# Optimization experiments

Measured on AMD Instinct MI355X. Metric: run time of the kernel, lower is better.

The kernel has to match this reference:

```python
import jax, jax.numpy as jnp
import numpy as np

N = 4_000_000

# AxisTypes: ZThenX=0, Bisector=1, ZBisect=2, ThreeFold=3, ZOnly=4, NoAxisType=5

def _normv(v):
    return v / jnp.linalg.norm(v, axis=-1, keepdims=True)


def _rot_matrices(coords, z_atoms, x_atoms, y_atoms, axis_types):
    # z axis: toward z neighbor
    z_vec = _normv(coords[z_atoms] - coords)  # (N,3)

    # x vector: gather-based for most types, synthetic for ZOnly/NoAxisType
    fz_only = (axis_types == 4) | (axis_types == 5)
    x_gather = _normv(coords[x_atoms] - coords)
    z0 = z_vec[:, 0:1]
    x_zonly = jnp.concatenate([1.0 - z0, z0, jnp.zeros_like(z0)], axis=1)
    x_vec = jnp.where(fz_only[:, None], x_zonly, x_gather)

    # Bisector: z <- normalize(z + x)
    fb = (axis_types == 1)[:, None]
    z_vec = jnp.where(fb, _normv(z_vec + x_vec), z_vec)

    # y-neighbor direction, used by ZBisect and ThreeFold
    y_nb = _normv(coords[y_atoms] - coords)

    # ZBisect: x <- normalize(x + y_nb)
    fzb = (axis_types == 2)[:, None]
    x_vec = jnp.where(fzb, _normv(x_vec + y_nb), x_vec)

    # ThreeFold: z <- normalize(z + x + y_nb)
    ftf = (axis_types == 3)[:, None]
    z_vec = jnp.where(ftf, _normv(z_vec + x_vec + y_nb), z_vec)

    # Gram-Schmidt orthogonalize x against z, y = z x x
    x_vec = _normv(x_vec - z_vec * jnp.sum(z_vec * x_vec, axis=1, keepdims=True))
    y_vec = jnp.cross(z_vec, x_vec)

    # NoAxisType: identity frame
    fna = (axis_types == 5)[:, None]
    ex = jnp.array([1.0, 0.0, 0.0], coords.dtype)
    ey = jnp.array([0.0, 1.0, 0.0], coords.dtype)
    ez = jnp.array([0.0, 0.0, 1.0], coords.dtype)
    x_vec = jnp.where(fna, ex, x_vec)
    y_vec = jnp.where(fna, ey, y_vec)
    z_vec = jnp.where(fna, ez, z_vec)

    # rows = local X, Y, Z in global coords -> (N,3,3)
    return jnp.stack([x_vec, y_vec, z_vec], axis=1)


def setup_inputs() -> dict:
    key = jax.random.key(0)
    k1, k2, k3, k4, k5, k6, k7 = jax.random.split(key, 7)
    coords = jax.random.normal(k1, (N, 3), jnp.float32) * 10.0
    idx = jnp.arange(N)
    # avoid self-index (zero vector -> NaN in normVec, same as torch original)
    z_atoms = (idx + jax.random.randint(k2, (N,), 1, N)) % N
    x_atoms = (idx + jax.random.randint(k3, (N,), 1, N)) % N
    y_atoms = (idx + jax.random.randint(k4, (N,), 1, N)) % N
    axis_types = jax.random.randint(k5, (N,), 0, 6)
    dipoles = jax.random.normal(k6, (N, 3), jnp.float32)
    quadrupoles = jax.random.normal(k7, (N, 3, 3), jnp.float32)
    return dict(coords=coords, z_atoms=z_atoms, x_atoms=x_atoms,
                y_atoms=y_atoms, axis_types=axis_types,
                dipoles=dipoles, quadrupoles=quadrupoles)


def reference(coords, z_atoms, x_atoms, y_atoms, axis_types, dipoles, quadrupoles):
    rot = _rot_matrices(coords, z_atoms, x_atoms, y_atoms, axis_types)  # (N,3,3)
    # torch: bmm(d.unsqueeze(1), rot).squeeze(1) -> d @ rot
    d = jnp.einsum('nk,nkj->nj', dipoles, rot)
    # torch: rot^T @ q @ rot
    q = jnp.einsum('nki,nkl,nlj->nij', rot, quadrupoles, rot)
    return (d, q)
```

## Files before the change

### kernel.cpp

```cpp
#include <hip/hip_runtime.h>


__device__ __forceinline__ float3 nrm3(float ax, float ay, float az) {
    float s = ax * ax + ay * ay + az * az;
    float r = 1.0f / sqrtf(s);
    return make_float3(ax * r, ay * r, az * r);
}

__device__ __forceinline__ void rot_matrix(
    int t, float cx, float cy, float cz,
    int zi, int xi, int yi,
    const float* __restrict__ coords,
    float R[9])
{
    if (t == 5) {
        R[0] = 1.0f; R[1] = 0.0f; R[2] = 0.0f;
        R[3] = 0.0f; R[4] = 1.0f; R[5] = 0.0f;
        R[6] = 0.0f; R[7] = 0.0f; R[8] = 1.0f;
        return;
    }

    float3 zv = nrm3(coords[3 * zi + 0] - cx,
                     coords[3 * zi + 1] - cy,
                     coords[3 * zi + 2] - cz);

    float3 xv;
    if (t == 4) {
        xv = make_float3(1.0f - zv.x, zv.x, 0.0f);
    } else {
        xv = nrm3(coords[3 * xi + 0] - cx,
                  coords[3 * xi + 1] - cy,
                  coords[3 * xi + 2] - cz);
    }

    if (t == 1) {
        zv = nrm3(zv.x + xv.x, zv.y + xv.y, zv.z + xv.z);
    }

    if (t == 2 || t == 3) {
        float3 yn = nrm3(coords[3 * yi + 0] - cx,
                         coords[3 * yi + 1] - cy,
                         coords[3 * yi + 2] - cz);
        if (t == 2) {
            xv = nrm3(xv.x + yn.x, xv.y + yn.y, xv.z + yn.z);
        } else {
            zv = nrm3(zv.x + xv.x + yn.x, zv.y + xv.y + yn.y, zv.z + xv.z + yn.z);
        }
    }

    float dzx = zv.x * xv.x + zv.y * xv.y + zv.z * xv.z;
    xv = nrm3(xv.x - zv.x * dzx, xv.y - zv.y * dzx, xv.z - zv.z * dzx);

    float3 yv = make_float3(zv.y * xv.z - zv.z * xv.y,
                            zv.z * xv.x - zv.x * xv.z,
                            zv.x * xv.y - zv.y * xv.x);

    R[0] = xv.x; R[1] = xv.y; R[2] = xv.z;
    R[3] = yv.x; R[4] = yv.y; R[5] = yv.z;
    R[6] = zv.x; R[7] = zv.y; R[8] = zv.z;
}

__device__ __forceinline__ void apply_rot(
    const float R[9], const float dp[3], const float Q[9],
    float od[3], float oq[9])
{
    od[0] = dp[0] * R[0] + dp[1] * R[3] + dp[2] * R[6];
    od[1] = dp[0] * R[1] + dp[1] * R[4] + dp[2] * R[7];
    od[2] = dp[0] * R[2] + dp[1] * R[5] + dp[2] * R[8];

    float M[9];
#pragma unroll
    for (int a = 0; a < 3; ++a) {
#pragma unroll
        for (int l = 0; l < 3; ++l) {
            M[a * 3 + l] = R[0 * 3 + a] * Q[0 * 3 + l]
                         + R[1 * 3 + a] * Q[1 * 3 + l]
                         + R[2 * 3 + a] * Q[2 * 3 + l];
        }
    }
#pragma unroll
    for (int a = 0; a < 3; ++a) {
#pragma unroll
        for (int b = 0; b < 3; ++b) {
            oq[a * 3 + b] = M[a * 3 + 0] * R[0 * 3 + b]
                          + M[a * 3 + 1] * R[1 * 3 + b]
                          + M[a * 3 + 2] * R[2 * 3 + b];
        }
    }
}

__global__ __launch_bounds__(256) void mp_rot4_kernel(
    const float* __restrict__ coords,
    const int* __restrict__ za,
    const int* __restrict__ xa,
    const int* __restrict__ ya,
    const int* __restrict__ at,
    const float* __restrict__ dip,
    const float* __restrict__ quad,
    float* __restrict__ out_d,
    float* __restrict__ out_q,
    int ngroups, int n)
{
    int g = blockIdx.x * blockDim.x + threadIdx.x;
    if (g >= ngroups) return;
    int base = 4 * g;

    if (base + 4 <= n) {
        float4 cA = ((const float4*)coords)[3 * g + 0];
        float4 cB = ((const float4*)coords)[3 * g + 1];
        float4 cC = ((const float4*)coords)[3 * g + 2];
        float c[12] = {cA.x, cA.y, cA.z, cA.w, cB.x, cB.y, cB.z, cB.w,
                       cC.x, cC.y, cC.z, cC.w};

        float4 dA = ((const float4*)dip)[3 * g + 0];
        float4 dB = ((const float4*)dip)[3 * g + 1];
        float4 dC = ((const float4*)dip)[3 * g + 2];
        float dp[12] = {dA.x, dA.y, dA.z, dA.w, dB.x, dB.y, dB.z, dB.w,
                        dC.x, dC.y, dC.z, dC.w};

        float q[36];
#pragma unroll
        for (int k = 0; k < 9; ++k) {
            float4 v = ((const float4*)quad)[9 * g + k];
            q[4 * k + 0] = v.x; q[4 * k + 1] = v.y;
            q[4 * k + 2] = v.z; q[4 * k + 3] = v.w;
        }

        int4 z4 = ((const int4*)za)[g];
        int4 x4 = ((const int4*)xa)[g];
        int4 y4 = ((const int4*)ya)[g];
        int4 t4 = ((const int4*)at)[g];
        int zi[4] = {z4.x, z4.y, z4.z, z4.w};
        int xi[4] = {x4.x, x4.y, x4.z, x4.w};
        int yi[4] = {y4.x, y4.y, y4.z, y4.w};
        int ti[4] = {t4.x, t4.y, t4.z, t4.w};

        float od[12], oq[36];
#pragma unroll
        for (int a = 0; a < 4; ++a) {
            float R[9];
            rot_matrix(ti[a], c[3 * a + 0], c[3 * a + 1], c[3 * a + 2],
                       zi[a], xi[a], yi[a], coords, R);
            apply_rot(R, &dp[3 * a], &q[9 * a], &od[3 * a], &oq[9 * a]);
        }

        ((float4*)out_d)[3 * g + 0] = make_float4(od[0], od[1], od[2], od[3]);
        ((float4*)out_d)[3 * g + 1] = make_float4(od[4], od[5], od[6], od[7]);
        ((float4*)out_d)[3 * g + 2] = make_float4(od[8], od[9], od[10], od[11]);
#pragma unroll
        for (int k = 0; k < 9; ++k) {
            ((float4*)out_q)[9 * g + k] =
                make_float4(oq[4 * k + 0], oq[4 * k + 1],
                            oq[4 * k + 2], oq[4 * k + 3]);
        }
    } else {
        for (int i = base; i < n; ++i) {
            float R[9];
            rot_matrix(at[i], coords[3 * i + 0], coords[3 * i + 1],
                       coords[3 * i + 2], za[i], xa[i], ya[i], coords, R);
            float dpl[3] = {dip[3 * i + 0], dip[3 * i + 1], dip[3 * i + 2]};
            float Q[9];
#pragma unroll
            for (int k = 0; k < 9; ++k) Q[k] = quad[9 * i + k];
            float od[3], oq[9];
            apply_rot(R, dpl, Q, od, oq);
#pragma unroll
            for (int k = 0; k < 3; ++k) out_d[3 * i + k] = od[k];
#pragma unroll
            for (int k = 0; k < 9; ++k) out_q[9 * i + k] = oq[k];
        }
    }
}

extern "C" void kernel_launch(void* const* d_in, const int* in_sizes, int n_in,
                              void* d_out, int out_size, void* d_ws, size_t ws_size,
                              hipStream_t stream) {
    const float* coords = (const float*)d_in[0];
    const int* za = (const int*)d_in[1];
    const int* xa = (const int*)d_in[2];
    const int* ya = (const int*)d_in[3];
    const int* at = (const int*)d_in[4];
    const float* dip = (const float*)d_in[5];
    const float* quad = (const float*)d_in[6];

    int n = in_sizes[1];
    float* out_d = (float*)d_out;
    float* out_q = out_d + (size_t)3 * n;

    int ngroups = (n + 3) / 4;
    int block = 256;
    int grid = (ngroups + block - 1) / block;
    mp_rot4_kernel<<<grid, block, 0, stream>>>(coords, za, xa, ya, at, dip, quad,
                                               out_d, out_q, ngroups, n);
}
```

Baseline: 212.3 us.

## Hoist neighbor gathers ahead of compute and use nontemporal streaming loads/stores

All random neighbor coordinate gathers for the four atoms are issued up front, before the dense dipole and quadrupole loads and any math, so the latency of many gathers overlaps. The y-neighbor gather is skipped for atom types that do not use it. Streaming inputs and outputs switch to nontemporal loads and stores so they do not pollute the cache that holds the randomly gathered coords. Issuing every gather early raises register pressure, which may reduce occupancy.

```diff
diff --git a/kernel.cpp b/kernel.cpp
--- a/kernel.cpp
+++ b/kernel.cpp
@@ -1,5 +1,8 @@
 #include <hip/hip_runtime.h>
 
+
+typedef float f32x4 __attribute__((ext_vector_type(4)));
+typedef int   i32x4 __attribute__((ext_vector_type(4)));
 
 __device__ __forceinline__ float3 nrm3(float ax, float ay, float az) {
     float s = ax * ax + ay * ay + az * az;
@@ -7,11 +10,8 @@
     return make_float3(ax * r, ay * r, az * r);
 }
 
-__device__ __forceinline__ void rot_matrix(
-    int t, float cx, float cy, float cz,
-    int zi, int xi, int yi,
-    const float* __restrict__ coords,
-    float R[9])
+__device__ __forceinline__ void rot_from_deltas(
+    int t, const float* dz, const float* dx, const float* dy, float R[9])
 {
     if (t == 5) {
         R[0] = 1.0f; R[1] = 0.0f; R[2] = 0.0f;
@@ -20,17 +20,13 @@
         return;
     }
 
-    float3 zv = nrm3(coords[3 * zi + 0] - cx,
-                     coords[3 * zi + 1] - cy,
-                     coords[3 * zi + 2] - cz);
+    float3 zv = nrm3(dz[0], dz[1], dz[2]);
 
     float3 xv;
     if (t == 4) {
         xv = make_float3(1.0f - zv.x, zv.x, 0.0f);
     } else {
-        xv = nrm3(coords[3 * xi + 0] - cx,
-                  coords[3 * xi + 1] - cy,
-                  coords[3 * xi + 2] - cz);
+        xv = nrm3(dx[0], dx[1], dx[2]);
     }
 
     if (t == 1) {
@@ -38,9 +34,7 @@
     }
 
     if (t == 2 || t == 3) {
-        float3 yn = nrm3(coords[3 * yi + 0] - cx,
-                         coords[3 * yi + 1] - cy,
-                         coords[3 * yi + 2] - cz);
+        float3 yn = nrm3(dy[0], dy[1], dy[2]);
         if (t == 2) {
             xv = nrm3(xv.x + yn.x, xv.y + yn.y, xv.z + yn.z);
         } else {
@@ -70,26 +64,22 @@
 
     float M[9];
 #pragma unroll
-    for (int a = 0; a < 3; ++a) {
-#pragma unroll
-        for (int l = 0; l < 3; ++l) {
+    for (int a = 0; a < 3; ++a)
+#pragma unroll
+        for (int l = 0; l < 3; ++l)
             M[a * 3 + l] = R[0 * 3 + a] * Q[0 * 3 + l]
                          + R[1 * 3 + a] * Q[1 * 3 + l]
                          + R[2 * 3 + a] * Q[2 * 3 + l];
-        }
-    }
-#pragma unroll
-    for (int a = 0; a < 3; ++a) {
-#pragma unroll
-        for (int b = 0; b < 3; ++b) {
+#pragma unroll
+    for (int a = 0; a < 3; ++a)
+#pragma unroll
+        for (int b = 0; b < 3; ++b)
             oq[a * 3 + b] = M[a * 3 + 0] * R[0 * 3 + b]
                           + M[a * 3 + 1] * R[1 * 3 + b]
                           + M[a * 3 + 2] * R[2 * 3 + b];
-        }
-    }
-}
-
-__global__ __launch_bounds__(256) void mp_rot4_kernel(
+}
+
+__global__ __launch_bounds__(256) void mp_rot4_nt_kernel(
     const float* __restrict__ coords,
     const int* __restrict__ za,
     const int* __restrict__ xa,
@@ -106,58 +96,97 @@
     int base = 4 * g;
 
     if (base + 4 <= n) {
-        float4 cA = ((const float4*)coords)[3 * g + 0];
-        float4 cB = ((const float4*)coords)[3 * g + 1];
-        float4 cC = ((const float4*)coords)[3 * g + 2];
-        float c[12] = {cA.x, cA.y, cA.z, cA.w, cB.x, cB.y, cB.z, cB.w,
-                       cC.x, cC.y, cC.z, cC.w};
-
-        float4 dA = ((const float4*)dip)[3 * g + 0];
-        float4 dB = ((const float4*)dip)[3 * g + 1];
-        float4 dC = ((const float4*)dip)[3 * g + 2];
-        float dp[12] = {dA.x, dA.y, dA.z, dA.w, dB.x, dB.y, dB.z, dB.w,
-                        dC.x, dC.y, dC.z, dC.w};
-
-        float q[36];
-#pragma unroll
-        for (int k = 0; k < 9; ++k) {
-            float4 v = ((const float4*)quad)[9 * g + k];
-            q[4 * k + 0] = v.x; q[4 * k + 1] = v.y;
-            q[4 * k + 2] = v.z; q[4 * k + 3] = v.w;
-        }
-
-        int4 z4 = ((const int4*)za)[g];
-        int4 x4 = ((const int4*)xa)[g];
-        int4 y4 = ((const int4*)ya)[g];
-        int4 t4 = ((const int4*)at)[g];
+        i32x4 z4 = __builtin_nontemporal_load((const i32x4*)za + g);
+        i32x4 x4 = __builtin_nontemporal_load((const i32x4*)xa + g);
+        i32x4 y4 = __builtin_nontemporal_load((const i32x4*)ya + g);
+        i32x4 t4 = __builtin_nontemporal_load((const i32x4*)at + g);
         int zi[4] = {z4.x, z4.y, z4.z, z4.w};
         int xi[4] = {x4.x, x4.y, x4.z, x4.w};
         int yi[4] = {y4.x, y4.y, y4.z, y4.w};
         int ti[4] = {t4.x, t4.y, t4.z, t4.w};
 
+        f32x4 cA = ((const f32x4*)coords)[3 * g + 0];
+        f32x4 cB = ((const f32x4*)coords)[3 * g + 1];
+        f32x4 cC = ((const f32x4*)coords)[3 * g + 2];
+        float c[12] = {cA.x, cA.y, cA.z, cA.w, cB.x, cB.y, cB.z, cB.w,
+                       cC.x, cC.y, cC.z, cC.w};
+
+        float gz[12], gx[12], gy[12];
+#pragma unroll
+        for (int a = 0; a < 4; ++a) {
+#pragma unroll
+            for (int k = 0; k < 3; ++k)
+                gz[3 * a + k] = coords[3 * zi[a] + k];
+        }
+#pragma unroll
+        for (int a = 0; a < 4; ++a) {
+#pragma unroll
+            for (int k = 0; k < 3; ++k)
+                gx[3 * a + k] = coords[3 * xi[a] + k];
+        }
+#pragma unroll
+        for (int a = 0; a < 4; ++a) {
+            bool needy = (ti[a] == 2) | (ti[a] == 3);
+            if (needy) {
+#pragma unroll
+                for (int k = 0; k < 3; ++k)
+                    gy[3 * a + k] = coords[3 * yi[a] + k];
+            } else {
+#pragma unroll
+                for (int k = 0; k < 3; ++k) gy[3 * a + k] = 0.0f;
+            }
+        }
+
+        f32x4 dA = __builtin_nontemporal_load((const f32x4*)dip + 3 * g + 0);
+        f32x4 dB = __builtin_nontemporal_load((const f32x4*)dip + 3 * g + 1);
+        f32x4 dC = __builtin_nontemporal_load((const f32x4*)dip + 3 * g + 2);
+        float dp[12] = {dA.x, dA.y, dA.z, dA.w, dB.x, dB.y, dB.z, dB.w,
+                        dC.x, dC.y, dC.z, dC.w};
+
+        float q[36];
+#pragma unroll
+        for (int k = 0; k < 9; ++k) {
+            f32x4 v = __builtin_nontemporal_load((const f32x4*)quad + 9 * g + k);
+            q[4 * k + 0] = v.x; q[4 * k + 1] = v.y;
+            q[4 * k + 2] = v.z; q[4 * k + 3] = v.w;
+        }
+
         float od[12], oq[36];
 #pragma unroll
         for (int a = 0; a < 4; ++a) {
+            float dz[3], dx[3], dy[3];
+#pragma unroll
+            for (int k = 0; k < 3; ++k) {
+                dz[k] = gz[3 * a + k] - c[3 * a + k];
+                dx[k] = gx[3 * a + k] - c[3 * a + k];
+                dy[k] = gy[3 * a + k] - c[3 * a + k];
+            }
             float R[9];
-            rot_matrix(ti[a], c[3 * a + 0], c[3 * a + 1], c[3 * a + 2],
-                       zi[a], xi[a], yi[a], coords, R);
+            rot_from_deltas(ti[a], dz, dx, dy, R);
             apply_rot(R, &dp[3 * a], &q[9 * a], &od[3 * a], &oq[9 * a]);
         }
 
-        ((float4*)out_d)[3 * g + 0] = make_float4(od[0], od[1], od[2], od[3]);
-        ((float4*)out_d)[3 * g + 1] = make_float4(od[4], od[5], od[6], od[7]);
-        ((float4*)out_d)[3 * g + 2] = make_float4(od[8], od[9], od[10], od[11]);
+        f32x4 odA = {od[0], od[1], od[2], od[3]};
+        f32x4 odB = {od[4], od[5], od[6], od[7]};
+        f32x4 odC = {od[8], od[9], od[10], od[11]};
+        __builtin_nontemporal_store(odA, (f32x4*)out_d + 3 * g + 0);
+        __builtin_nontemporal_store(odB, (f32x4*)out_d + 3 * g + 1);
+        __builtin_nontemporal_store(odC, (f32x4*)out_d + 3 * g + 2);
 #pragma unroll
         for (int k = 0; k < 9; ++k) {
-            ((float4*)out_q)[9 * g + k] =
-                make_float4(oq[4 * k + 0], oq[4 * k + 1],
-                            oq[4 * k + 2], oq[4 * k + 3]);
+            f32x4 v = {oq[4 * k + 0], oq[4 * k + 1], oq[4 * k + 2], oq[4 * k + 3]};
+            __builtin_nontemporal_store(v, (f32x4*)out_q + 9 * g + k);
         }
     } else {
         for (int i = base; i < n; ++i) {
+            int t = at[i];
+            float cx = coords[3 * i + 0], cy = coords[3 * i + 1], cz = coords[3 * i + 2];
+            int zi = za[i], xi = xa[i], yi = ya[i];
+            float dz[3] = {coords[3 * zi + 0] - cx, coords[3 * zi + 1] - cy, coords[3 * zi + 2] - cz};
+            float dx[3] = {coords[3 * xi + 0] - cx, coords[3 * xi + 1] - cy, coords[3 * xi + 2] - cz};
+            float dy[3] = {coords[3 * yi + 0] - cx, coords[3 * yi + 1] - cy, coords[3 * yi + 2] - cz};
             float R[9];
-            rot_matrix(at[i], coords[3 * i + 0], coords[3 * i + 1],
-                       coords[3 * i + 2], za[i], xa[i], ya[i], coords, R);
+            rot_from_deltas(t, dz, dx, dy, R);
             float dpl[3] = {dip[3 * i + 0], dip[3 * i + 1], dip[3 * i + 2]};
             float Q[9];
 #pragma unroll
@@ -190,6 +219,6 @@
     int ngroups = (n + 3) / 4;
     int block = 256;
     int grid = (ngroups + block - 1) / block;
-    mp_rot4_kernel<<<grid, block, 0, stream>>>(coords, za, xa, ya, at, dip, quad,
-                                               out_d, out_q, ngroups, n);
-}
+    mp_rot4_nt_kernel<<<grid, block, 0, stream>>>(coords, za, xa, ya, at, dip, quad,
+                                                  out_d, out_q, ngroups, n);
+}
```

Result: slower. 431.6 us (+103.3%).
